# Performance work log

Hardware: AMD Instinct MI355X
Metric: run time of the kernel (lower is better)

The kernel has to match this reference:

```python
import jax, jax.numpy as jnp
import numpy as np

N = 100000   # nodes
E = 1600000  # edges
IN = 64
HID = 64
C = 2
EPS = 1e-12


def _linear_init(k, fan_in, fan_out):
    s = 1.0 / np.sqrt(fan_in)
    kw, kb = jax.random.split(k)
    w = jax.random.uniform(kw, (fan_in, fan_out), minval=-s, maxval=s, dtype=jnp.float32)
    b = jax.random.uniform(kb, (fan_out,), minval=-s, maxval=s, dtype=jnp.float32)
    return w, b


def setup_inputs() -> dict:
    key = jax.random.key(0)
    ks = jax.random.split(key, 12)
    x = jax.random.normal(ks[0], (N, IN), dtype=jnp.float32)
    edge_index = jax.random.randint(ks[1], (2, E), 0, N, dtype=jnp.int64)
    w1, b1 = _linear_init(ks[2], IN, HID)
    w2, b2 = _linear_init(ks[3], HID, HID)
    w3, b3 = _linear_init(ks[4], HID, HID)
    wg1, bg1 = _linear_init(ks[5], HID, HID)   # GCNConv 1
    wg2, bg2 = _linear_init(ks[6], HID, HID)   # GCNConv 2
    beta = jnp.ones((), dtype=jnp.float32)     # AGNN learnable scalar
    wf, bf = _linear_init(ks[7], HID, HID)     # W_f
    wx, bx = _linear_init(ks[8], HID, HID)     # W_x
    wc, bc = _linear_init(ks[9], 2 * HID, C)   # classifier
    return {"x": x, "edge_index": edge_index,
            "w1": w1, "b1": b1, "w2": w2, "b2": b2, "w3": w3, "b3": b3,
            "wg1": wg1, "bg1": bg1, "wg2": wg2, "bg2": bg2, "beta": beta,
            "wf": wf, "bf": bf, "wx": wx, "bx": bx, "wc": wc, "bc": bc}


def _segment_softmax(logits, seg, n):
    m = jax.ops.segment_max(logits, seg, num_segments=n)
    e = jnp.exp(logits - m[seg])
    s = jax.ops.segment_sum(e, seg, num_segments=n)
    return e / s[seg]


def _gcn_conv(x, w, b, row, col, norm):
    # x' = D^{-1/2}(A+I)D^{-1/2} x W + b  (PyG GCNConv with self-loops)
    h = x @ w                                   # [N, HID]
    msg = h[row] * norm[:, None]                # gather + scale  [E+N, HID]
    out = jax.ops.segment_sum(msg, col, num_segments=N)
    return out + b


def _agnn_conv(x, beta, row, col):
    # cosine-similarity attention (PyG AGNNConv), self-loops included
    xn = x / (jnp.linalg.norm(x, axis=-1, keepdims=True) + EPS)
    alpha = beta * jnp.sum(xn[row] * xn[col], axis=-1)   # [E+N]
    a = _segment_softmax(alpha, col, N)
    return jax.ops.segment_sum(a[:, None] * x[row], col, num_segments=N)


def reference(x, edge_index, w1, b1, w2, b2, w3, b3, wg1, bg1, wg2, bg2,
              beta, wf, bf, wx, bx, wc, bc):
    # add self-loops
    loop = jnp.arange(N, dtype=edge_index.dtype)
    row = jnp.concatenate([edge_index[0], loop])
    col = jnp.concatenate([edge_index[1], loop])
    # symmetric GCN normalization
    deg = jax.ops.segment_sum(jnp.ones_like(col, dtype=jnp.float32), col, num_segments=N)
    dinv = jnp.where(deg > 0, deg ** -0.5, 0.0)
    norm = dinv[row] * dinv[col]

    # input MLP
    h = jax.nn.relu(x @ w1 + b1)
    h = jax.nn.relu(h @ w2 + b2)
    h = h @ w3 + b3                              # [N, HID]

    f0 = _gcn_conv(h, wg1, bg1, row, col, norm)
    f1 = _gcn_conv(h, wg2, bg2, row, col, norm)
    h1 = _agnn_conv(h, beta, row, col)

    h_filters = jnp.stack([f0, f1], axis=1)      # [N, 2, HID]
    h_proj = jnp.tanh(h_filters @ wf + bf)       # [N, 2, HID]
    x_proj = jnp.tanh(h @ wx + bx)               # [N, HID]
    logit = jnp.einsum('nkh,nh->nk', h_proj, x_proj)   # bmm -> [N, 2]
    score = jax.nn.softmax(logit, axis=1)
    res = jnp.einsum('nkh,nk->nh', h_filters, score)   # attention-weighted fusion
    res = jnp.concatenate([res, h1], axis=1)     # [N, 2*HID]
    y_hat = res @ wc + bc                        # dropout disabled (eval)
    return y_hat
```

## Files before the change

### kernel.cpp

```cpp
#include <hip/hip_runtime.h>
#include <math.h>


#define SCT 8192

typedef float v2f __attribute__((ext_vector_type(2)));

__device__ __forceinline__ v2f v2fma(v2f a, v2f b, v2f c) {
#if __has_builtin(__builtin_elementwise_fma)
    return __builtin_elementwise_fma(a, b, c);
#else
    v2f r; r.x = fmaf(a.x, b.x, c.x); r.y = fmaf(a.y, b.y, c.y); return r;
#endif
}

__device__ __forceinline__ void lds_fence() {
    asm volatile("s_waitcnt lgkmcnt(0)" ::: "memory");
}

__device__ __forceinline__ float fast_tanh(float x) {
    x = fminf(fmaxf(x, -15.f), 15.f);
    float e = __expf(2.f * x);
    return (e - 1.f) * __frcp_rn(e + 1.f);
}

__device__ __forceinline__ void load_rows32(const float* __restrict__ src, int row0, int n,
                                            float (*dst)[68], int t)
{
    int e = t * 8;
    int r = e >> 6, i = e & 63;
    int grow = row0 + r;
    float4 v0 = make_float4(0.f, 0.f, 0.f, 0.f), v1 = v0;
    if (grow < n) {
        const float* p = src + (size_t)grow * 64 + i;
        v0 = *(const float4*)p;
        v1 = *(const float4*)(p + 4);
    }
    *(float4*)&dst[r][i]     = v0;
    *(float4*)&dst[r][i + 4] = v1;
}

__device__ __forceinline__ void gemm_core_pk(const float (*in)[68], const float* w,
                                             const float* b, int rg, int cg,
                                             float (&o0)[4], float (&o1)[4])
{
    float bb0 = b[4*cg], bb1 = b[4*cg+1], bb2 = b[4*cg+2], bb3 = b[4*cg+3];
    v2f acc0a = {bb0, bb1}, acc0b = {bb2, bb3};
    v2f acc1a = acc0a, acc1b = acc0b;
    const int r0 = 2 * rg, r1 = 2 * rg + 1;
#pragma unroll
    for (int i = 0; i < 64; i += 4) {
        float4 a0 = *(const float4*)&in[r0][i];
        float4 a1 = *(const float4*)&in[r1][i];
        const float* q = &w[i * 64 + 4 * cg];
        v2f q0a = *(const v2f*)(q),       q0b = *(const v2f*)(q + 2);
        v2f q1a = *(const v2f*)(q + 64),  q1b = *(const v2f*)(q + 66);
        v2f q2a = *(const v2f*)(q + 128), q2b = *(const v2f*)(q + 130);
        v2f q3a = *(const v2f*)(q + 192), q3b = *(const v2f*)(q + 194);
        v2f s;
        s = (v2f){a0.x, a0.x}; acc0a = v2fma(s, q0a, acc0a); acc0b = v2fma(s, q0b, acc0b);
        s = (v2f){a0.y, a0.y}; acc0a = v2fma(s, q1a, acc0a); acc0b = v2fma(s, q1b, acc0b);
        s = (v2f){a0.z, a0.z}; acc0a = v2fma(s, q2a, acc0a); acc0b = v2fma(s, q2b, acc0b);
        s = (v2f){a0.w, a0.w}; acc0a = v2fma(s, q3a, acc0a); acc0b = v2fma(s, q3b, acc0b);
        s = (v2f){a1.x, a1.x}; acc1a = v2fma(s, q0a, acc1a); acc1b = v2fma(s, q0b, acc1b);
        s = (v2f){a1.y, a1.y}; acc1a = v2fma(s, q1a, acc1a); acc1b = v2fma(s, q1b, acc1b);
        s = (v2f){a1.z, a1.z}; acc1a = v2fma(s, q2a, acc1a); acc1b = v2fma(s, q2b, acc1b);
        s = (v2f){a1.w, a1.w}; acc1a = v2fma(s, q3a, acc1a); acc1b = v2fma(s, q3b, acc1b);
    }
    o0[0] = acc0a.x; o0[1] = acc0a.y; o0[2] = acc0b.x; o0[3] = acc0b.y;
    o1[0] = acc1a.x; o1[1] = acc1a.y; o1[2] = acc1b.x; o1[3] = acc1b.y;
}

__device__ __forceinline__ void gemm4_pk(const float (*in)[68], const float* __restrict__ w,
                                         const float* b, int rgs, int cg,
                                         float (&out)[4][4])
{
    float bb0 = b[4*cg], bb1 = b[4*cg+1], bb2 = b[4*cg+2], bb3 = b[4*cg+3];
    v2f ba = {bb0, bb1}, bbv = {bb2, bb3};
    v2f acc[4][2];
#pragma unroll
    for (int r = 0; r < 4; r++) { acc[r][0] = ba; acc[r][1] = bbv; }
    const float* wp = w + 4 * cg;
    const int r0 = 4 * rgs;
#pragma unroll 2
    for (int i = 0; i < 64; i += 4) {
        v2f q0a = *(const v2f*)(wp + (i + 0) * 64), q0b = *(const v2f*)(wp + (i + 0) * 64 + 2);
        v2f q1a = *(const v2f*)(wp + (i + 1) * 64), q1b = *(const v2f*)(wp + (i + 1) * 64 + 2);
        v2f q2a = *(const v2f*)(wp + (i + 2) * 64), q2b = *(const v2f*)(wp + (i + 2) * 64 + 2);
        v2f q3a = *(const v2f*)(wp + (i + 3) * 64), q3b = *(const v2f*)(wp + (i + 3) * 64 + 2);
#pragma unroll
        for (int r = 0; r < 4; r++) {
            float4 a = *(const float4*)&in[r0 + r][i];
            v2f s;
            s = (v2f){a.x, a.x}; acc[r][0] = v2fma(s, q0a, acc[r][0]); acc[r][1] = v2fma(s, q0b, acc[r][1]);
            s = (v2f){a.y, a.y}; acc[r][0] = v2fma(s, q1a, acc[r][0]); acc[r][1] = v2fma(s, q1b, acc[r][1]);
            s = (v2f){a.z, a.z}; acc[r][0] = v2fma(s, q2a, acc[r][0]); acc[r][1] = v2fma(s, q2b, acc[r][1]);
            s = (v2f){a.w, a.w}; acc[r][0] = v2fma(s, q3a, acc[r][0]); acc[r][1] = v2fma(s, q3b, acc[r][1]);
        }
    }
#pragma unroll
    for (int r = 0; r < 4; r++) {
        out[r][0] = acc[r][0].x; out[r][1] = acc[r][0].y;
        out[r][2] = acc[r][1].x; out[r][3] = acc[r][1].y;
    }
}


__global__ __launch_bounds__(256) void k_zero(int* __restrict__ arr, int n1)
{
    int i = blockIdx.x * 256 + threadIdx.x;
    if (i < n1) arr[i] = 0;
}

__global__ __launch_bounds__(256) void k_bhist(const int* __restrict__ col,
                                               int* __restrict__ bhist, int e)
{
    __shared__ int hist[256];
    int t = threadIdx.x;
    hist[t] = 0;
    __syncthreads();
    int base = blockIdx.x * SCT;
    int end = min(e, base + SCT);
    for (int i = base + t; i < end; i += 256)
        atomicAdd(&hist[col[i] >> 9], 1);
    __syncthreads();
    if (hist[t]) atomicAdd(&bhist[t], hist[t]);
}

__global__ __launch_bounds__(256) void k_bscan(const int* __restrict__ bhist,
                                               int* __restrict__ bbase, int* __restrict__ bcur)
{
    __shared__ int s[256];
    int t = threadIdx.x;
    int v = bhist[t];
    s[t] = v;
    __syncthreads();
    for (int d = 1; d < 256; d <<= 1) {
        int u = (t >= d) ? s[t - d] : 0;
        __syncthreads();
        s[t] += u;
        __syncthreads();
    }
    int b = s[t] - v;
    bbase[t] = b;
    bcur[t] = b;
}

__global__ __launch_bounds__(256) void k_bscatter2(const int* __restrict__ row,
    const int* __restrict__ col, int* __restrict__ bcur,
    int2* __restrict__ pairs, int e, int nbk)
{
    __shared__ int hist[256], lcur[256], gb[256], s[256];
    __shared__ int2 buf[SCT];
    int t = threadIdx.x;
    int base = blockIdx.x * SCT;
    int end = min(e, base + SCT);
    hist[t] = 0;
    __syncthreads();
    for (int i = base + t; i < end; i += 256)
        atomicAdd(&hist[col[i] >> 9], 1);
    __syncthreads();
    int v = hist[t];
    s[t] = v;
    __syncthreads();
    for (int d = 1; d < 256; d <<= 1) {
        int u = (t >= d) ? s[t - d] : 0;
        __syncthreads();
        s[t] += u;
        __syncthreads();
    }
    lcur[t] = s[t] - v;
    __syncthreads();
    for (int i = base + t; i < end; i += 256) {
        int c = col[i];
        int slot = atomicAdd(&lcur[c >> 9], 1);
        buf[slot] = make_int2(row[i], c);
    }
    if (v > 0) gb[t] = atomicAdd(&bcur[t], v);
    __syncthreads();
    int wv = t >> 6, lane = t & 63;
    for (int b = wv; b < nbk; b += 4) {
        int cnt = hist[b];
        if (cnt == 0) continue;
        int lo = s[b] - cnt;
        int go = gb[b];
        for (int j = lane; j < cnt; j += 64)
            pairs[go + j] = buf[lo + j];
    }
}

__global__ __launch_bounds__(256) void k_fill3(const int2* __restrict__ pairs,
    const int* __restrict__ bbase, const int* __restrict__ bhist,
    int* __restrict__ arr, int* __restrict__ csr, int n)
{
    __shared__ int nh[512], nc[512], s[256];
    int b = blockIdx.x, t = threadIdx.x;
    int pbase = bbase[b];
    int cnt = bhist[b];
    int nodebase = b << 9;
    nh[t] = 0; nh[t + 256] = 0;
    __syncthreads();
    for (int i = t; i < cnt; i += 256)
        atomicAdd(&nh[pairs[pbase + i].y - nodebase], 1);
    __syncthreads();
    int v0 = nh[2 * t], v1 = nh[2 * t + 1];
    int sum = v0 + v1;
    s[t] = sum;
    __syncthreads();
    for (int d = 1; d < 256; d <<= 1) {
        int u = (t >= d) ? s[t - d] : 0;
        __syncthreads();
        s[t] += u;
        __syncthreads();
    }
    int excl = s[t] - sum;
    int n0 = nodebase + 2 * t, n1 = n0 + 1;
    nc[2 * t]     = pbase + excl;
    nc[2 * t + 1] = pbase + excl + v0;
    if (n0 < n) arr[n0] = pbase + excl + v0;
    if (n1 < n) arr[n1] = pbase + excl + v0 + v1;
    __syncthreads();
    for (int i = t; i < cnt; i += 256) {
        int2 pr = pairs[pbase + i];
        int p = atomicAdd(&nc[pr.y - nodebase], 1);
        csr[p] = pr.x;
    }
}


__global__ __launch_bounds__(256) void k_pre(
    const float* __restrict__ wg1, const float* __restrict__ bg1,
    const float* __restrict__ wg2, const float* __restrict__ bg2,
    const float* __restrict__ wf,  const float* __restrict__ bf,
    const float* __restrict__ wc,  float* __restrict__ pre)
{
    __shared__ float wfs[4096];
    __shared__ float wcs[128];
    int t = threadIdx.x;
    for (int i = t; i < 4096; i += 256) wfs[i] = wf[i];
    if (t < 128) wcs[t] = wc[t];
    __syncthreads();
    int i = t & 63, jb = (t >> 6) * 16;
    float acc0[16], acc1[16];
#pragma unroll
    for (int j = 0; j < 16; j++) { acc0[j] = 0.f; acc1[j] = 0.f; }
#pragma unroll 1
    for (int k = 0; k < 64; k++) {
        float a = wg1[i * 64 + k];
        float b = wg2[i * 64 + k];
#pragma unroll
        for (int j = 0; j < 16; j++) {
            float w = wfs[k * 64 + jb + j];
            acc0[j] = fmaf(a, w, acc0[j]);
            acc1[j] = fmaf(b, w, acc1[j]);
        }
    }
#pragma unroll
    for (int j = 0; j < 16; j++) {
        pre[i * 64 + jb + j]        = acc0[j];
        pre[4096 + i * 64 + jb + j] = acc1[j];
    }
    if (t < 64) {
        float s0 = bf[t], s1 = bf[t];
#pragma unroll 1
        for (int m = 0; m < 64; m++) {
            s0 = fmaf(bg1[m], wfs[m * 64 + t], s0);
            s1 = fmaf(bg2[m], wfs[m * 64 + t], s1);
        }
        pre[8192 + t] = s0;
        pre[8256 + t] = s1;
        float u00 = 0.f, u01 = 0.f, u10 = 0.f, u11 = 0.f;
#pragma unroll 1
        for (int m = 0; m < 64; m++) {
            float g1 = wg1[t * 64 + m], g2 = wg2[t * 64 + m];
            u00 = fmaf(g1, wcs[m * 2 + 0], u00);
            u01 = fmaf(g1, wcs[m * 2 + 1], u01);
            u10 = fmaf(g2, wcs[m * 2 + 0], u10);
            u11 = fmaf(g2, wcs[m * 2 + 1], u11);
        }
        pre[8320 + t * 2]     = u00;
        pre[8320 + t * 2 + 1] = u01;
        pre[8448 + t * 2]     = u10;
        pre[8448 + t * 2 + 1] = u11;
    }
    if (t == 0) {
        float v00 = 0.f, v01 = 0.f, v10 = 0.f, v11 = 0.f;
#pragma unroll 1
        for (int m = 0; m < 64; m++) {
            v00 = fmaf(bg1[m], wcs[m * 2 + 0], v00);
            v01 = fmaf(bg1[m], wcs[m * 2 + 1], v01);
            v10 = fmaf(bg2[m], wcs[m * 2 + 0], v10);
            v11 = fmaf(bg2[m], wcs[m * 2 + 1], v11);
        }
        pre[8576] = v00; pre[8577] = v01; pre[8578] = v10; pre[8579] = v11;
    }
}


__global__ __launch_bounds__(256) void k_mlp(const float* __restrict__ x,
    const float* __restrict__ w1, const float* __restrict__ b1,
    const float* __restrict__ w2, const float* __restrict__ b2,
    const float* __restrict__ w3, const float* __restrict__ b3,
    const int* __restrict__ arr, float* __restrict__ h,
    float2* __restrict__ nrm2, int n)
{
    __shared__ float b1s[64], b2s[64], b3s[64];
    __shared__ float xs[4][16][68];
    int t = threadIdx.x;
    if (t < 64) { b1s[t] = b1[t]; b2s[t] = b2[t]; b3s[t] = b3[t]; }
    __syncthreads();
    int wv = t >> 6, lane = t & 63;
    int cg = lane & 15, rgs = lane >> 4;
    int row0 = blockIdx.x * 64 + wv * 16;
    float (*ws)[68] = xs[wv];

    {
        int r = lane >> 2, c = (lane & 3) * 16;
        int grow = row0 + r;
        float4 v0 = make_float4(0.f,0.f,0.f,0.f), v1 = v0, v2 = v0, v3 = v0;
        if (grow < n) {
            const float* p = x + (size_t)grow * 64 + c;
            v0 = *(const float4*)p;       v1 = *(const float4*)(p + 4);
            v2 = *(const float4*)(p + 8); v3 = *(const float4*)(p + 12);
        }
        *(float4*)&ws[r][c]      = v0; *(float4*)&ws[r][c + 4]  = v1;
        *(float4*)&ws[r][c + 8]  = v2; *(float4*)&ws[r][c + 12] = v3;
    }
    lds_fence();

    float acc[4][4];
    gemm4_pk(ws, w1, b1s, rgs, cg, acc);
    lds_fence();
#pragma unroll
    for (int r = 0; r < 4; r++)
        *(float4*)&ws[4 * rgs + r][4 * cg] =
            make_float4(fmaxf(acc[r][0], 0.f), fmaxf(acc[r][1], 0.f),
                        fmaxf(acc[r][2], 0.f), fmaxf(acc[r][3], 0.f));
    lds_fence();
    gemm4_pk(ws, w2, b2s, rgs, cg, acc);
    lds_fence();
#pragma unroll
    for (int r = 0; r < 4; r++)
        *(float4*)&ws[4 * rgs + r][4 * cg] =
            make_float4(fmaxf(acc[r][0], 0.f), fmaxf(acc[r][1], 0.f),
                        fmaxf(acc[r][2], 0.f), fmaxf(acc[r][3], 0.f));
    lds_fence();
    gemm4_pk(ws, w3, b3s, rgs, cg, acc);

    int r0g = row0 + 4 * rgs;
    float sr[4];
#pragma unroll
    for (int r = 0; r < 4; r++) {
        int grow = r0g + r;
        if (grow < n)
            *(float4*)&h[(size_t)grow * 64 + 4 * cg] =
                make_float4(acc[r][0], acc[r][1], acc[r][2], acc[r][3]);
        sr[r] = acc[r][0]*acc[r][0] + acc[r][1]*acc[r][1]
              + acc[r][2]*acc[r][2] + acc[r][3]*acc[r][3];
    }
#pragma unroll
    for (int d = 1; d < 16; d <<= 1) {
#pragma unroll
        for (int r = 0; r < 4; r++) sr[r] += __shfl_xor(sr[r], d, 64);
    }
    if (cg == 0) {
#pragma unroll
        for (int r = 0; r < 4; r++) {
            int grow = r0g + r;
            if (grow < n) {
                int st = (grow == 0) ? 0 : arr[grow - 1];
                nrm2[grow] = make_float2(1.0f / (sqrtf(sr[r]) + 1e-12f),
                                         rsqrtf((float)(arr[grow] - st + 1)));
            }
        }
    }
}


__global__ __launch_bounds__(256) void k_gather(const float* __restrict__ h,
    const int* __restrict__ arr, const int* __restrict__ csr,
    const float2* __restrict__ nrm2, const float* __restrict__ beta_p,
    const float* __restrict__ wc,
    float* __restrict__ agg, float2* __restrict__ yp, int n)
{
    __shared__ float reda[4][4][2][66];
    __shared__ float redn[4][4][2][66];
    int wv = threadIdx.x >> 6;
    int lane = threadIdx.x & 63;
    int sub = lane >> 5;
    int l32 = lane & 31;
    int g = l32 >> 3, s = l32 & 7;
    int base = sub << 5;
    int node = blockIdx.x * 8 + wv * 2 + sub;
    bool valid = node < n;
    int nd = valid ? node : 0;
    float beta = beta_p[0];
    const char* hb = (const char*)h;

    unsigned selfoff = ((unsigned)nd << 8) + ((unsigned)s << 5);
    float4 hA = *(const float4*)(hb + selfoff);
    float4 hB = *(const float4*)(hb + selfoff + 16);
    v2f hc0 = {hA.x, hA.y}, hc1 = {hA.z, hA.w};
    v2f hc2 = {hB.x, hB.y}, hc3 = {hB.z, hB.w};

    v2f sv = hc0 * hc0;
    sv = v2fma(hc1, hc1, sv); sv = v2fma(hc2, hc2, sv); sv = v2fma(hc3, hc3, sv);
    float ss = sv.x + sv.y;
#pragma unroll
    for (int d = 1; d < 8; d <<= 1) ss += __shfl_xor(ss, d, 64);
    float2 ncv = nrm2[nd];
    float rnc = ncv.x, dc = ncv.y;
    float brn = beta * rnc;
    float wself = __expf(brn * ss * rnc);

    v2f a0 = {0.f,0.f}, a1 = {0.f,0.f}, a2 = {0.f,0.f}, a3 = {0.f,0.f};
    v2f n0 = {0.f,0.f}, n1 = {0.f,0.f}, n2 = {0.f,0.f}, n3 = {0.f,0.f};
    float denom = 0.f;
    if (g == 0) {
        v2f dcv = {dc, dc}, wsv = {wself, wself};
        a0 = dcv * hc0; a1 = dcv * hc1; a2 = dcv * hc2; a3 = dcv * hc3;
        n0 = wsv * hc0; n1 = wsv * hc1; n2 = wsv * hc2; n3 = wsv * hc3;
        denom = wself;
    }

    int start = (!valid || nd == 0) ? 0 : arr[nd - 1];
    int end = valid ? arr[nd] : 0;
#pragma unroll 1
    for (int k0 = start; k0 < end; k0 += 32) {
        int m = min(32, end - k0);
        int idx = 0; float rv = 0.f, dv = 0.f;
        if (l32 < m) {
            idx = csr[k0 + l32];
            float2 ndv = nrm2[idx];
            rv = ndv.x; dv = ndv.y;
        }
        int ei = __shfl(idx, base + g, 64);
        unsigned eoff = ((unsigned)ei << 8) + ((unsigned)s << 5);
        float4 cA = *(const float4*)(hb + eoff);
        float4 cB = *(const float4*)(hb + eoff + 16);
#pragma unroll 1
        for (int k = 0; k < m; k += 4) {
            float4 fA = cA, fB = cB;
            if (k + 4 < m) {
                int e2 = __shfl(idx, base + k + 4 + g, 64);
                unsigned off2 = ((unsigned)e2 << 8) + ((unsigned)s << 5);
                cA = *(const float4*)(hb + off2);
                cB = *(const float4*)(hb + off2 + 16);
            }
            float rnr = __shfl(rv, base + k + g, 64);
            float dvr = __shfl(dv, base + k + g, 64);
            v2f f0 = {fA.x, fA.y}, f1 = {fA.z, fA.w};
            v2f f2 = {fB.x, fB.y}, f3 = {fB.z, fB.w};
            v2f ps = f0 * hc0;
            ps = v2fma(f1, hc1, ps); ps = v2fma(f2, hc2, ps); ps = v2fma(f3, hc3, ps);
            float p = ps.x + ps.y;
#pragma unroll
            for (int d = 1; d < 8; d <<= 1) p += __shfl_xor(p, d, 64);
            bool act = (k + g) < m;
            float w   = act ? __expf(brn * p * rnr) : 0.f;
            float dve = act ? dvr : 0.f;
            v2f wsp = {w, w}, dsp = {dve, dve};
            a0 = v2fma(dsp, f0, a0); a1 = v2fma(dsp, f1, a1);
            a2 = v2fma(dsp, f2, a2); a3 = v2fma(dsp, f3, a3);
            n0 = v2fma(wsp, f0, n0); n1 = v2fma(wsp, f1, n1);
            n2 = v2fma(wsp, f2, n2); n3 = v2fma(wsp, f3, n3);
            denom += w;
        }
    }

    {
        float* wa = &reda[wv][g][sub][8 * s];
        float* wn = &redn[wv][g][sub][8 * s];
        *(float4*)wa       = make_float4(a0.x, a0.y, a1.x, a1.y);
        *(float4*)(wa + 4) = make_float4(a2.x, a2.y, a3.x, a3.y);
        *(float4*)wn       = make_float4(n0.x, n0.y, n1.x, n1.y);
        *(float4*)(wn + 4) = make_float4(n2.x, n2.y, n3.x, n3.y);
    }
    lds_fence();
    float a_lo, a_hi, n_lo, n_hi;
    {
        const float* r0p = &reda[wv][0][sub][0];
        const float* r1p = &redn[wv][0][sub][0];
        float t0 = r0p[l32]       + r0p[132 + l32];
        float t1 = r0p[264 + l32] + r0p[396 + l32];
        float t2 = r0p[l32 + 32]       + r0p[132 + l32 + 32];
        float t3 = r0p[264 + l32 + 32] + r0p[396 + l32 + 32];
        a_lo = t0 + t1; a_hi = t2 + t3;
        float u0 = r1p[l32]       + r1p[132 + l32];
        float u1 = r1p[264 + l32] + r1p[396 + l32];
        float u2 = r1p[l32 + 32]       + r1p[132 + l32 + 32];
        float u3 = r1p[264 + l32 + 32] + r1p[396 + l32 + 32];
        n_lo = u0 + u1; n_hi = u2 + u3;
    }
    if (valid) {
        agg[(size_t)node * 64 + l32]      = dc * a_lo;
        agg[(size_t)node * 64 + l32 + 32] = dc * a_hi;
    }

    denom += __shfl_xor(denom, 8, 64);
    denom += __shfl_xor(denom, 16, 64);

    float2 w_lo = *(const float2*)(wc + 128 + 2 * l32);
    float2 w_hi = *(const float2*)(wc + 128 + 2 * (l32 + 32));
    float cx = n_lo * w_lo.x + n_hi * w_hi.x;
    float cy = n_lo * w_lo.y + n_hi * w_hi.y;
#pragma unroll
    for (int d = 1; d < 32; d <<= 1) { cx += __shfl_xor(cx, d, 64); cy += __shfl_xor(cy, d, 64); }
    if (l32 == 0 && valid) {
        float inv = 1.0f / denom;
        yp[node] = make_float2(cx * inv, cy * inv);
    }
}


__global__ __launch_bounds__(256) void k_epi(const float* __restrict__ agg,
    const float* __restrict__ hbuf, const float2* __restrict__ yp,
    const float* __restrict__ pre, const float* __restrict__ wx,
    const float* __restrict__ bx, const float* __restrict__ bc,
    float* __restrict__ y, int n, int ntiles)
{
    __shared__ float W0s[4096], W1s[4096], wxs[4096];
    __shared__ float c0s[64], c1s[64], bxs[64], us[256], vs[4], bcs[2];
    __shared__ float A[32][68], H[32][68];
    int t = threadIdx.x;
    for (int i = t; i < 4096; i += 256) { W0s[i] = pre[i]; W1s[i] = pre[4096 + i]; wxs[i] = wx[i]; }
    if (t < 64) { c0s[t] = pre[8192 + t]; c1s[t] = pre[8256 + t]; bxs[t] = bx[t]; }
    us[t] = pre[8320 + t];
    if (t < 4) vs[t] = pre[8576 + t];
    if (t < 2) bcs[t] = bc[t];
    __syncthreads();
    int cg = t & 15, rg = t >> 4;
    for (int tile = blockIdx.x; tile < ntiles; tile += gridDim.x) {
        int row0 = tile * 32;
        load_rows32(agg,  row0, n, A, t);
        load_rows32(hbuf, row0, n, H, t);
        __syncthreads();
        int r0g = row0 + 2 * rg, r1g = r0g + 1;
        float xp0[4], xp1[4];
        gemm_core_pk(H, wxs, bxs, rg, cg, xp0, xp1);
#pragma unroll
        for (int j = 0; j < 4; j++) { xp0[j] = fast_tanh(xp0[j]); xp1[j] = fast_tanh(xp1[j]); }
        float a0[4], a1[4];
        gemm_core_pk(A, W0s, c0s, rg, cg, a0, a1);
        float l00 = 0.f, l01 = 0.f;
#pragma unroll
        for (int j = 0; j < 4; j++) {
            l00 = fmaf(fast_tanh(a0[j]), xp0[j], l00);
            l01 = fmaf(fast_tanh(a1[j]), xp1[j], l01);
        }
        gemm_core_pk(A, W1s, c1s, rg, cg, a0, a1);
        float l10 = 0.f, l11 = 0.f;
#pragma unroll
        for (int j = 0; j < 4; j++) {
            l10 = fmaf(fast_tanh(a0[j]), xp0[j], l10);
            l11 = fmaf(fast_tanh(a1[j]), xp1[j], l11);
        }
        float4 av0 = *(const float4*)&A[2 * rg][4 * cg];
        float4 av1 = *(const float4*)&A[2 * rg + 1][4 * cg];
        float za0=0.f, za1=0.f, zb0=0.f, zb1=0.f;
        float zc0=0.f, zc1=0.f, zd0=0.f, zd1=0.f;
#pragma unroll
        for (int j = 0; j < 4; j++) {
            int k = 4 * cg + j;
            float u0c0 = us[k * 2], u0c1 = us[k * 2 + 1];
            float u1c0 = us[128 + k * 2], u1c1 = us[128 + k * 2 + 1];
            float p0 = (&av0.x)[j], p1 = (&av1.x)[j];
            za0 = fmaf(p0, u0c0, za0); za1 = fmaf(p0, u0c1, za1);
            zb0 = fmaf(p0, u1c0, zb0); zb1 = fmaf(p0, u1c1, zb1);
            zc0 = fmaf(p1, u0c0, zc0); zc1 = fmaf(p1, u0c1, zc1);
            zd0 = fmaf(p1, u1c0, zd0); zd1 = fmaf(p1, u1c1, zd1);
        }
#pragma unroll
        for (int d = 1; d < 16; d <<= 1) {
            l00 += __shfl_xor(l00, d, 64); l01 += __shfl_xor(l01, d, 64);
            l10 += __shfl_xor(l10, d, 64); l11 += __shfl_xor(l11, d, 64);
            za0 += __shfl_xor(za0, d, 64); za1 += __shfl_xor(za1, d, 64);
            zb0 += __shfl_xor(zb0, d, 64); zb1 += __shfl_xor(zb1, d, 64);
            zc0 += __shfl_xor(zc0, d, 64); zc1 += __shfl_xor(zc1, d, 64);
            zd0 += __shfl_xor(zd0, d, 64); zd1 += __shfl_xor(zd1, d, 64);
        }
        if (cg == 0) {
            if (r0g < n) {
                float mx = fmaxf(l00, l10);
                float e0 = __expf(l00 - mx), e1 = __expf(l10 - mx);
                float inv = 1.0f / (e0 + e1);
                float s0 = e0 * inv, s1 = e1 * inv;
                float2 ypv = yp[r0g];
                float y0v = s0 * (za0 + vs[0]) + s1 * (zb0 + vs[2]) + ypv.x + bcs[0];
                float y1v = s0 * (za1 + vs[1]) + s1 * (zb1 + vs[3]) + ypv.y + bcs[1];
                *(float2*)&y[(size_t)r0g * 2] = make_float2(y0v, y1v);
            }
            if (r1g < n) {
                float mx = fmaxf(l01, l11);
                float e0 = __expf(l01 - mx), e1 = __expf(l11 - mx);
                float inv = 1.0f / (e0 + e1);
                float s0 = e0 * inv, s1 = e1 * inv;
                float2 ypv = yp[r1g];
                float y0v = s0 * (zc0 + vs[0]) + s1 * (zd0 + vs[2]) + ypv.x + bcs[0];
                float y1v = s0 * (zc1 + vs[1]) + s1 * (zd1 + vs[3]) + ypv.y + bcs[1];
                *(float2*)&y[(size_t)r1g * 2] = make_float2(y0v, y1v);
            }
        }
        __syncthreads();
    }
}

extern "C" void kernel_launch(void* const* d_in, const int* in_sizes, int n_in,
                              void* d_out, int out_size, void* d_ws, size_t ws_size,
                              hipStream_t stream)
{
    const float* x    = (const float*)d_in[0];
    const int*   ei   = (const int*)d_in[1];
    const float* w1   = (const float*)d_in[2];
    const float* b1   = (const float*)d_in[3];
    const float* w2   = (const float*)d_in[4];
    const float* b2   = (const float*)d_in[5];
    const float* w3   = (const float*)d_in[6];
    const float* b3   = (const float*)d_in[7];
    const float* wg1  = (const float*)d_in[8];
    const float* bg1  = (const float*)d_in[9];
    const float* wg2  = (const float*)d_in[10];
    const float* bg2  = (const float*)d_in[11];
    const float* beta = (const float*)d_in[12];
    const float* wf   = (const float*)d_in[13];
    const float* bf   = (const float*)d_in[14];
    const float* wx   = (const float*)d_in[15];
    const float* bx   = (const float*)d_in[16];
    const float* wc   = (const float*)d_in[17];
    const float* bc   = (const float*)d_in[18];
    float* y = (float*)d_out;

    int n = in_sizes[0] / 64;
    int e = in_sizes[1] / 2;
    const int* row = ei;
    const int* col = ei + e;

    char* p = (char*)d_ws;
    auto alloc = [&](size_t bytes) { char* q = p; p += (bytes + 255) & ~(size_t)255; return q; };
    float*  h    = (float*)alloc((size_t)n * 64 * 4);
    int*    csr  = (int*)alloc((size_t)e * 4);
    float2* nrm2 = (float2*)alloc((size_t)n * 8);
    int*    arr  = (int*)alloc((size_t)(n + 1) * 4);
    float2* yp   = (float2*)alloc((size_t)n * 8);
    float*  pre  = (float*)alloc(8704 * 4);
    int*    bhist = (int*)alloc(256 * 4);
    int*    bbase = (int*)alloc(256 * 4);
    int*    bcur  = (int*)alloc(256 * 4);

    int2* pairs = (int2*)h;
    float* agg = (float*)d_in[0];

    int ntiles = (n + 31) / 32;
    int ntile64 = (n + 63) / 64;
    int nbk = (n + 511) >> 9;
    int nsct = (e + SCT - 1) / SCT;

    k_pre<<<1, 256, 0, stream>>>(wg1, bg1, wg2, bg2, wf, bf, wc, pre);
    k_zero<<<1, 256, 0, stream>>>(bhist, 256);
    k_bhist<<<nsct, 256, 0, stream>>>(col, bhist, e);
    k_bscan<<<1, 256, 0, stream>>>(bhist, bbase, bcur);
    k_bscatter2<<<nsct, 256, 0, stream>>>(row, col, bcur, pairs, e, nbk);
    k_fill3<<<nbk, 256, 0, stream>>>(pairs, bbase, bhist, arr, csr, n);
    k_mlp<<<ntile64, 256, 0, stream>>>(x, w1, b1, w2, b2, w3, b3, arr, h, nrm2, n);
    k_gather<<<(n + 7) / 8, 256, 0, stream>>>(h, arr, csr, nrm2, beta, wc, agg, yp, n);
    k_epi<<<1024, 256, 0, stream>>>(agg, h, yp, pre, wx, bx, bc, y, n, ntiles);
}
```

Baseline: 374.6 us.

## Pack bucketed edge pairs into 32-bit words and cache them in LDS

The bucket scatter now writes one 32-bit word per edge: the 17-bit source row plus the 9-bit destination offset within its 512-node bucket, instead of an int2 pair. This halves the bytes written and read for the pairs buffer. The fill kernel caches up to 12288 packed pairs in shared memory on its first pass so the second pass can skip rereading global memory. The scatter chunk size shrinks so the packed LDS buffer stays small, and a zeroing kernel is replaced with hipMemsetAsync. The packing assumes node ids fit in 17 bits, which holds only while N stays below 131072, and the large LDS buffer may lower occupancy in the fill kernel.

```diff
diff --git a/kernel.cpp b/kernel.cpp
--- a/kernel.cpp
+++ b/kernel.cpp
@@ -2,7 +2,8 @@
 #include <math.h>
 
 
-#define SCT 8192
+#define SCT 6272
+#define F3CAP 12288
 
 typedef float v2f __attribute__((ext_vector_type(2)));
 
@@ -106,12 +107,6 @@
 }
 
 
-__global__ __launch_bounds__(256) void k_zero(int* __restrict__ arr, int n1)
-{
-    int i = blockIdx.x * 256 + threadIdx.x;
-    if (i < n1) arr[i] = 0;
-}
-
 __global__ __launch_bounds__(256) void k_bhist(const int* __restrict__ col,
                                                int* __restrict__ bhist, int e)
 {
@@ -148,10 +143,10 @@
 
 __global__ __launch_bounds__(256) void k_bscatter2(const int* __restrict__ row,
     const int* __restrict__ col, int* __restrict__ bcur,
-    int2* __restrict__ pairs, int e, int nbk)
+    unsigned* __restrict__ pairs, int e, int nbk)
 {
     __shared__ int hist[256], lcur[256], gb[256], s[256];
-    __shared__ int2 buf[SCT];
+    __shared__ unsigned buf[SCT];
     int t = threadIdx.x;
     int base = blockIdx.x * SCT;
     int end = min(e, base + SCT);
@@ -174,7 +169,7 @@
     for (int i = base + t; i < end; i += 256) {
         int c = col[i];
         int slot = atomicAdd(&lcur[c >> 9], 1);
-        buf[slot] = make_int2(row[i], c);
+        buf[slot] = (unsigned)row[i] | ((unsigned)(c & 511) << 17);
     }
     if (v > 0) gb[t] = atomicAdd(&bcur[t], v);
     __syncthreads();
@@ -189,19 +184,23 @@
     }
 }
 
-__global__ __launch_bounds__(256) void k_fill3(const int2* __restrict__ pairs,
+__global__ __launch_bounds__(256) void k_fill3(const unsigned* __restrict__ pairs,
     const int* __restrict__ bbase, const int* __restrict__ bhist,
     int* __restrict__ arr, int* __restrict__ csr, int n)
 {
     __shared__ int nh[512], nc[512], s[256];
+    __shared__ unsigned sbuf[F3CAP];
     int b = blockIdx.x, t = threadIdx.x;
     int pbase = bbase[b];
     int cnt = bhist[b];
     int nodebase = b << 9;
     nh[t] = 0; nh[t + 256] = 0;
     __syncthreads();
-    for (int i = t; i < cnt; i += 256)
-        atomicAdd(&nh[pairs[pbase + i].y - nodebase], 1);
+    for (int i = t; i < cnt; i += 256) {
+        unsigned pv = pairs[pbase + i];
+        if (i < F3CAP) sbuf[i] = pv;
+        atomicAdd(&nh[pv >> 17], 1);
+    }
     __syncthreads();
     int v0 = nh[2 * t], v1 = nh[2 * t + 1];
     int sum = v0 + v1;
@@ -221,9 +220,9 @@
     if (n1 < n) arr[n1] = pbase + excl + v0 + v1;
     __syncthreads();
     for (int i = t; i < cnt; i += 256) {
-        int2 pr = pairs[pbase + i];
-        int p = atomicAdd(&nc[pr.y - nodebase], 1);
-        csr[p] = pr.x;
+        unsigned pv = (i < F3CAP) ? sbuf[i] : pairs[pbase + i];
+        int p = atomicAdd(&nc[pv >> 17], 1);
+        csr[p] = (int)(pv & 0x1FFFFu);
     }
 }
 
@@ -647,7 +646,7 @@
     int*    bbase = (int*)alloc(256 * 4);
     int*    bcur  = (int*)alloc(256 * 4);
 
-    int2* pairs = (int2*)h;
+    unsigned* pairs = (unsigned*)h;
     float* agg = (float*)d_in[0];
 
     int ntiles = (n + 31) / 32;
@@ -656,7 +655,7 @@
     int nsct = (e + SCT - 1) / SCT;
 
     k_pre<<<1, 256, 0, stream>>>(wg1, bg1, wg2, bg2, wf, bf, wc, pre);
-    k_zero<<<1, 256, 0, stream>>>(bhist, 256);
+    hipMemsetAsync(bhist, 0, 256 * sizeof(int), stream);
     k_bhist<<<nsct, 256, 0, stream>>>(col, bhist, e);
     k_bscan<<<1, 256, 0, stream>>>(bhist, bbase, bcur);
     k_bscatter2<<<nsct, 256, 0, stream>>>(row, col, bcur, pairs, e, nbk);
```

Result: no change. 370.5 us, median of 2 (-1.1%).
